# Kernel tuning notes

Hardware: AMD Instinct MI355X
Metric: run time of the kernel (lower is better)

## Reference

```python
import jax, jax.numpy as jnp
import numpy as np

B, T, F, H, S = 4096, 256, 64, 128, 32


def setup_inputs() -> dict:
    key = jax.random.key(0)
    ks = jax.random.split(key, 10)
    return {
        "x": jax.random.normal(ks[0], (B, T, F), jnp.float32),
        "static": jax.random.normal(ks[1], (B, S), jnp.float32),
        "hs0": jax.random.normal(ks[2], (B, H), jnp.float32),
        "cs0": jax.random.normal(ks[3], (B, H), jnp.float32),
        "W_ih": jax.random.normal(ks[4], (4 * H, F), jnp.float32) * 0.1,
        "W_hh": jax.random.normal(ks[5], (4 * H, H), jnp.float32) * 0.1,
        "b_ih": jax.random.normal(ks[6], (4 * H,), jnp.float32) * 0.1,
        "b_hh": jax.random.normal(ks[7], (4 * H,), jnp.float32) * 0.1,
        "W_lin": jax.random.normal(ks[8], (1, H + S), jnp.float32) * 0.1,
        "b_lin": jax.random.normal(ks[9], (1,), jnp.float32) * 0.1,
    }


def reference(x, static, hs0, cs0, W_ih, W_hh, b_ih, b_hh, W_lin, b_lin):
    # x: [B, T, F] -> time-major [T, B, F]; precompute input projections for all steps
    xs = jnp.swapaxes(x, 0, 1)
    px = jnp.einsum('tbf,gf->tbg', xs, W_ih) + b_ih  # [T, B, 4H]

    def step(carry, px_t):
        h, c = carry
        gates = px_t + h @ W_hh.T + b_hh  # [B, 4H]
        i, f, g, o = jnp.split(gates, 4, axis=-1)  # PyTorch LSTM gate order
        i = jax.nn.sigmoid(i)
        f = jax.nn.sigmoid(f)
        g = jnp.tanh(g)
        o = jax.nn.sigmoid(o)
        c = f * c + i * g
        h = o * jnp.tanh(c)
        return (h, c), None

    (h, c), _ = jax.lax.scan(step, (hs0, cs0), px)
    full = jnp.concatenate([h, static], axis=1)  # [B, H+S]
    return full @ W_lin.T + b_lin  # [B, 1]
```

## Files before the change

### kernel.cpp

```cpp
#include <hip/hip_runtime.h>
#include <hip/hip_bf16.h>

#define B_ 4096
#define T_ 256
#define F_ 64
#define H_ 128
#define S_ 32

typedef __attribute__((ext_vector_type(8))) short bf16x8;
typedef __attribute__((ext_vector_type(4))) float f32x4;

#define K1f (-1.4426950408889634f)
#define K2f (-2.8853900817779268f)

#define MF(A, B, C) __builtin_amdgcn_mfma_f32_16x16x32_bf16((A), (B), (C), 0, 0, 0)

__device__ __forceinline__ float bf2f(unsigned short u) {
    unsigned v = (unsigned)u << 16;
    return __builtin_bit_cast(float, v);
}
__device__ __forceinline__ short f2bs(float f) {
    return (short)__bfloat16_as_ushort(__float2bfloat16(f));
}

#define PHASE(HR, HW, XW, XN, TLD)                                               \
  {                                                                              \
    const char* hr_ = (const char*)(HR);                                         \
    bf16x8 a0 = *(const bf16x8*)(hr_ + fh0);                                     \
    bf16x8 a1 = *(const bf16x8*)(hr_ + fh1);                                     \
    bf16x8 a2 = *(const bf16x8*)(hr_ + fh2);                                     \
    bf16x8 a3 = *(const bf16x8*)(hr_ + fh3);                                     \
                    \
    { __hip_bfloat162 qx = __float22bfloat162_rn(xheld);                         \
      *(__hip_bfloat162*)((char*)(XW) + xws) = qx; }                             \
    xheld = *(const float2*)(gxs + (size_t)(TLD) * F_);                          \
                                          \
    f32x4 ac0 = sd0, ac1 = sd1, ac2 = sd2, ac3 = sd3;                            \
    ac0 = MF(wf[0][2], a0, ac0); ac1 = MF(wf[1][2], a0, ac1);                    \
    ac2 = MF(wf[2][2], a0, ac2); ac3 = MF(wf[3][2], a0, ac3);                    \
    ac0 = MF(wf[0][3], a1, ac0); ac1 = MF(wf[1][3], a1, ac1);                    \
    ac2 = MF(wf[2][3], a1, ac2); ac3 = MF(wf[3][3], a1, ac3);                    \
    ac0 = MF(wf[0][4], a2, ac0); ac1 = MF(wf[1][4], a2, ac1);                    \
    ac2 = MF(wf[2][4], a2, ac2); ac3 = MF(wf[3][4], a2, ac3);                    \
    ac0 = MF(wf[0][5], a3, ac0); ac1 = MF(wf[1][5], a3, ac1);                    \
    ac2 = MF(wf[2][5], a3, ac2); ac3 = MF(wf[3][5], a3, ac3);                    \
                                  \
    float hn[4];                                                                 \
    _Pragma("unroll")                                                            \
    for (int q = 0; q < 4; ++q) {                                                \
      const float ea = __builtin_amdgcn_exp2f(__builtin_fmaf(ac0[q], K1f, bs0[q])); \
      const float ef = __builtin_amdgcn_exp2f(__builtin_fmaf(ac1[q], K1f, bs1[q])); \
      const float eg = __builtin_amdgcn_exp2f(__builtin_fmaf(ac2[q], K2f, btn[q])); \
      const float eo = __builtin_amdgcn_exp2f(__builtin_fmaf(ac3[q], K1f, bs3[q])); \
      const float r1 = __builtin_amdgcn_rcpf(1.0f + ef);                         \
      const float r2 = __builtin_amdgcn_rcpf((1.0f + ea) * (1.0f + eg));         \
      const float cn = __builtin_fmaf(c[q], r1, (1.0f - eg) * r2);               \
      c[q] = cn;                                                                 \
      const float cc = fmaxf(cn, -30.0f);                                        \
      const float ec = __builtin_amdgcn_exp2f(cc * K2f);                         \
      const float r3 = __builtin_amdgcn_rcpf((1.0f + eo) * (1.0f + ec));         \
      hn[q] = (1.0f - ec) * r3;                                                  \
    }                                                                            \
    { float2 p0; p0.x = hn[0]; p0.y = hn[1];                                     \
      float2 p1; p1.x = hn[2]; p1.y = hn[3];                                     \
      __hip_bfloat162 b01 = __float22bfloat162_rn(p0);                           \
      __hip_bfloat162 b23 = __float22bfloat162_rn(p1);                           \
      uint2 uv; uv.x = *(unsigned*)&b01; uv.y = *(unsigned*)&b23;                \
      *(uint2*)((char*)(HW) + hwb) = uv; }                                       \
              \
    { const char* xn_ = (const char*)(XN);                                       \
      bf16x8 nf0 = *(const bf16x8*)(xn_ + fx0);                                  \
      bf16x8 nf1 = *(const bf16x8*)(xn_ + fx1);                                  \
      sd0 = MF(wf[0][0], nf0, z4); sd1 = MF(wf[1][0], nf0, z4);                  \
      sd2 = MF(wf[2][0], nf0, z4); sd3 = MF(wf[3][0], nf0, z4);                  \
      sd0 = MF(wf[0][1], nf1, sd0); sd1 = MF(wf[1][1], nf1, sd1);                \
      sd2 = MF(wf[2][1], nf1, sd2); sd3 = MF(wf[3][1], nf1, sd3); }              \
    asm volatile("s_waitcnt lgkmcnt(0)" ::: "memory");                           \
    __builtin_amdgcn_s_barrier();                                                \
  }

__global__ __launch_bounds__(512, 2) void lstm_fused_kernel(
    const float* __restrict__ x,
    const float* __restrict__ statik,
    const float* __restrict__ hs0,
    const float* __restrict__ cs0,
    const float* __restrict__ W_ih,
    const float* __restrict__ W_hh,
    const float* __restrict__ b_ih,
    const float* __restrict__ b_hh,
    const float* __restrict__ W_lin,
    const float* __restrict__ b_lin,
    float* __restrict__ out)
{
    __shared__ __align__(16) unsigned short h_l[2][16 * 128];
    __shared__ __align__(16) unsigned short x_l[4][16 * 64];

    const int tid  = threadIdx.x;
    const int lane = tid & 63;
    const int w    = tid >> 6;
    const int b0   = blockIdx.x * 16;

    if (w >= 4) __builtin_amdgcn_s_setprio(1);

    const int lrow = lane & 15;
    const int lkb  = lane >> 4;
    const int n0q  = w * 16 + lkb * 4;

    bf16x8 wf[4][6];
    #pragma unroll
    for (int g = 0; g < 4; ++g) {
        const int n = g * 128 + w * 16 + lrow;
        #pragma unroll
        for (int kt = 0; kt < 6; ++kt) {
            const int k0 = kt * 32 + lkb * 8;
            const float* src = (kt < 2) ? (W_ih + n * F_ + k0)
                                        : (W_hh + n * H_ + (k0 - 64));
            const float4 s0 = *(const float4*)(src);
            const float4 s1 = *(const float4*)(src + 4);
            bf16x8 v;
            v[0] = f2bs(s0.x); v[1] = f2bs(s0.y); v[2] = f2bs(s0.z); v[3] = f2bs(s0.w);
            v[4] = f2bs(s1.x); v[5] = f2bs(s1.y); v[6] = f2bs(s1.z); v[7] = f2bs(s1.w);
            wf[g][kt] = v;
        }
    }

    float bs0[4], bs1[4], btn[4], bs3[4];
    #pragma unroll
    for (int g = 0; g < 4; ++g) {
        const float4 bi = *(const float4*)(b_ih + g * 128 + n0q);
        const float4 bh = *(const float4*)(b_hh + g * 128 + n0q);
        const float bq[4] = {bi.x + bh.x, bi.y + bh.y, bi.z + bh.z, bi.w + bh.w};
        #pragma unroll
        for (int q = 0; q < 4; ++q) {
            if (g == 0)      bs0[q] = bq[q] * K1f;
            else if (g == 1) bs1[q] = bq[q] * K1f;
            else if (g == 2) btn[q] = bq[q] * K2f;
            else             bs3[q] = bq[q] * K1f;
        }
    }

    float c[4];
    {
        const float4 cv = *(const float4*)(cs0 + (size_t)(b0 + lrow) * H_ + n0q);
        c[0] = cv.x; c[1] = cv.y; c[2] = cv.z; c[3] = cv.w;
    }

    const int fsw = (lrow & 7) << 4;
    const int fx0 = lrow * 128 + ((lkb * 16) ^ fsw);
    const int fx1 = lrow * 128 + ((64 + lkb * 16) ^ fsw);
    const int fh0 = lrow * 256 + ((0   + lkb * 16) ^ fsw);
    const int fh1 = lrow * 256 + ((64  + lkb * 16) ^ fsw);
    const int fh2 = lrow * 256 + ((128 + lkb * 16) ^ fsw);
    const int fh3 = lrow * 256 + ((192 + lkb * 16) ^ fsw);
    const int hwb = lrow * 256 + ((n0q * 2) ^ fsw);

    const int srow = tid >> 5;
    const int scp  = tid & 31;
    const int ssw  = (srow & 7) << 4;
    const int xws  = srow * 128 + ((scp * 4) ^ ssw);

    const float* gxs = x + (size_t)(b0 + srow) * (T_ * F_) + scp * 2;
    float2 xheld;
    {
        const float* hp = hs0 + (size_t)(b0 + srow) * H_ + scp * 2;
        const float2 hv0 = *(const float2*)(hp);
        const float2 hv1 = *(const float2*)(hp + 64);
        __hip_bfloat162 q0 = __float22bfloat162_rn(hv0);
        __hip_bfloat162 q1 = __float22bfloat162_rn(hv1);
        *(__hip_bfloat162*)((char*)h_l[0] + srow * 256 + ((scp * 4) ^ ssw))       = q0;
        *(__hip_bfloat162*)((char*)h_l[0] + srow * 256 + ((128 + scp * 4) ^ ssw)) = q1;

        const float2 x0 = *(const float2*)(gxs);
        const float2 x1 = *(const float2*)(gxs + F_);
        __hip_bfloat162 qa = __float22bfloat162_rn(x0);
        __hip_bfloat162 qb = __float22bfloat162_rn(x1);
        *(__hip_bfloat162*)((char*)x_l[0] + xws) = qa;
        *(__hip_bfloat162*)((char*)x_l[1] + xws) = qb;
        xheld = *(const float2*)(gxs + 2 * F_);
    }
    __syncthreads();

    const f32x4 z4 = {0.0f, 0.0f, 0.0f, 0.0f};

    f32x4 sd0, sd1, sd2, sd3;
    {
        const char* xn_ = (const char*)x_l[0];
        bf16x8 nf0 = *(const bf16x8*)(xn_ + fx0);
        bf16x8 nf1 = *(const bf16x8*)(xn_ + fx1);
        sd0 = MF(wf[0][0], nf0, z4); sd1 = MF(wf[1][0], nf0, z4);
        sd2 = MF(wf[2][0], nf0, z4); sd3 = MF(wf[3][0], nf0, z4);
        sd0 = MF(wf[0][1], nf1, sd0); sd1 = MF(wf[1][1], nf1, sd1);
        sd2 = MF(wf[2][1], nf1, sd2); sd3 = MF(wf[3][1], nf1, sd3);
    }

    for (int t = 0; t < T_; t += 4) {
        const int t3 = (t + 3 < T_) ? t + 3 : T_ - 1;
        const int t4 = (t + 4 < T_) ? t + 4 : T_ - 1;
        const int t5 = (t + 5 < T_) ? t + 5 : T_ - 1;
        const int t6 = (t + 6 < T_) ? t + 6 : T_ - 1;
        PHASE(h_l[0], h_l[1], x_l[2], x_l[1], t3);
        PHASE(h_l[1], h_l[0], x_l[3], x_l[2], t4);
        PHASE(h_l[0], h_l[1], x_l[0], x_l[3], t5);
        PHASE(h_l[1], h_l[0], x_l[1], x_l[0], t6);
    }

    __builtin_amdgcn_s_setprio(0);

    {
        const char* hf = (const char*)h_l[0];
        const float wl0 = W_lin[lane];
        const float wl1 = W_lin[64 + lane];
        const float wl2 = (lane < S_) ? W_lin[128 + lane] : 0.0f;
        const float bl  = b_lin[0];
        #pragma unroll
        for (int rr = 0; rr < 2; ++rr) {
            const int r  = w * 2 + rr;
            const int rs = (r & 7) << 4;
            const unsigned short h0 =
                *(const unsigned short*)(hf + r * 256 + ((2 * lane) ^ rs));
            const unsigned short h1 =
                *(const unsigned short*)(hf + r * 256 + ((128 + 2 * lane) ^ rs));
            float p = bf2f(h0) * wl0 + bf2f(h1) * wl1;
            if (lane < S_) p += statik[(size_t)(b0 + r) * S_ + lane] * wl2;
            #pragma unroll
            for (int m = 32; m > 0; m >>= 1) p += __shfl_xor(p, m, 64);
            if (lane == 0) out[b0 + r] = p + bl;
        }
    }
}

extern "C" void kernel_launch(void* const* d_in, const int* in_sizes, int n_in,
                              void* d_out, int out_size, void* d_ws, size_t ws_size,
                              hipStream_t stream) {
    const float* x     = (const float*)d_in[0];
    const float* st    = (const float*)d_in[1];
    const float* hs0   = (const float*)d_in[2];
    const float* cs0   = (const float*)d_in[3];
    const float* W_ih  = (const float*)d_in[4];
    const float* W_hh  = (const float*)d_in[5];
    const float* b_ih  = (const float*)d_in[6];
    const float* b_hh  = (const float*)d_in[7];
    const float* W_lin = (const float*)d_in[8];
    const float* b_lin = (const float*)d_in[9];
    float* out = (float*)d_out;

    lstm_fused_kernel<<<dim3(B_ / 16), dim3(512), 0, stream>>>(
        x, st, hs0, cs0, W_ih, W_hh, b_ih, b_hh, W_lin, b_lin, out);
}
```

Measured before the change: 246.9 us.

## Split warps into two phase orderings to stagger MFMA and activation work

Waves 0-3 keep the original order (h MFMAs, activations, then next-step x seeds), while waves 4-7 compute the next-step x seed MFMAs first, before the h MFMAs and activations. The wave priority boost for the upper half is dropped. The aim is for the two groups of waves to hit the matrix unit and the transcendental/VALU work at different times within each barrier interval, so the pipes are shared better. It costs an extra set of four accumulator registers for the odd path and duplicates the loop code, which may add register pressure at 512 threads and 2 blocks per CU.

After: 261.5 us. 5.9% more time.

```diff
diff --git a/kernel.cpp b/kernel.cpp
--- a/kernel.cpp
+++ b/kernel.cpp
@@ -23,61 +23,86 @@
     return (short)__bfloat16_as_ushort(__float2bfloat16(f));
 }
 
-#define PHASE(HR, HW, XW, XN, TLD)                                               \
-  {                                                                              \
-    const char* hr_ = (const char*)(HR);                                         \
-    bf16x8 a0 = *(const bf16x8*)(hr_ + fh0);                                     \
-    bf16x8 a1 = *(const bf16x8*)(hr_ + fh1);                                     \
-    bf16x8 a2 = *(const bf16x8*)(hr_ + fh2);                                     \
-    bf16x8 a3 = *(const bf16x8*)(hr_ + fh3);                                     \
-                    \
-    { __hip_bfloat162 qx = __float22bfloat162_rn(xheld);                         \
-      *(__hip_bfloat162*)((char*)(XW) + xws) = qx; }                             \
-    xheld = *(const float2*)(gxs + (size_t)(TLD) * F_);                          \
-                                          \
-    f32x4 ac0 = sd0, ac1 = sd1, ac2 = sd2, ac3 = sd3;                            \
-    ac0 = MF(wf[0][2], a0, ac0); ac1 = MF(wf[1][2], a0, ac1);                    \
-    ac2 = MF(wf[2][2], a0, ac2); ac3 = MF(wf[3][2], a0, ac3);                    \
-    ac0 = MF(wf[0][3], a1, ac0); ac1 = MF(wf[1][3], a1, ac1);                    \
-    ac2 = MF(wf[2][3], a1, ac2); ac3 = MF(wf[3][3], a1, ac3);                    \
-    ac0 = MF(wf[0][4], a2, ac0); ac1 = MF(wf[1][4], a2, ac1);                    \
-    ac2 = MF(wf[2][4], a2, ac2); ac3 = MF(wf[3][4], a2, ac3);                    \
-    ac0 = MF(wf[0][5], a3, ac0); ac1 = MF(wf[1][5], a3, ac1);                    \
-    ac2 = MF(wf[2][5], a3, ac2); ac3 = MF(wf[3][5], a3, ac3);                    \
-                                  \
-    float hn[4];                                                                 \
-    _Pragma("unroll")                                                            \
-    for (int q = 0; q < 4; ++q) {                                                \
+
+#define STAGE_X(XW, TLD) \
+    { __hip_bfloat162 qx_ = __float22bfloat162_rn(xheld); \
+      *(__hip_bfloat162*)((char*)(XW) + xws) = qx_; } \
+    xheld = *(const float2*)(gxs + (size_t)(TLD) * F_);
+
+#define HMFMA16() \
+    ac0 = MF(wf[0][2], a0, ac0); ac1 = MF(wf[1][2], a0, ac1); \
+    ac2 = MF(wf[2][2], a0, ac2); ac3 = MF(wf[3][2], a0, ac3); \
+    ac0 = MF(wf[0][3], a1, ac0); ac1 = MF(wf[1][3], a1, ac1); \
+    ac2 = MF(wf[2][3], a1, ac2); ac3 = MF(wf[3][3], a1, ac3); \
+    ac0 = MF(wf[0][4], a2, ac0); ac1 = MF(wf[1][4], a2, ac1); \
+    ac2 = MF(wf[2][4], a2, ac2); ac3 = MF(wf[3][4], a2, ac3); \
+    ac0 = MF(wf[0][5], a3, ac0); ac1 = MF(wf[1][5], a3, ac1); \
+    ac2 = MF(wf[2][5], a3, ac2); ac3 = MF(wf[3][5], a3, ac3);
+
+#define SEEDS8(D0, D1, D2, D3, XN) \
+    { const char* xn_ = (const char*)(XN); \
+      bf16x8 nf0 = *(const bf16x8*)(xn_ + fx0); \
+      bf16x8 nf1 = *(const bf16x8*)(xn_ + fx1); \
+      D0 = MF(wf[0][0], nf0, z4);  D1 = MF(wf[1][0], nf0, z4); \
+      D2 = MF(wf[2][0], nf0, z4);  D3 = MF(wf[3][0], nf0, z4); \
+      D0 = MF(wf[0][1], nf1, D0);  D1 = MF(wf[1][1], nf1, D1); \
+      D2 = MF(wf[2][1], nf1, D2);  D3 = MF(wf[3][1], nf1, D3); }
+
+#define ACT_WRITE(HW) \
+    { float hn[4]; \
+    _Pragma("unroll") \
+    for (int q = 0; q < 4; ++q) { \
       const float ea = __builtin_amdgcn_exp2f(__builtin_fmaf(ac0[q], K1f, bs0[q])); \
       const float ef = __builtin_amdgcn_exp2f(__builtin_fmaf(ac1[q], K1f, bs1[q])); \
       const float eg = __builtin_amdgcn_exp2f(__builtin_fmaf(ac2[q], K2f, btn[q])); \
       const float eo = __builtin_amdgcn_exp2f(__builtin_fmaf(ac3[q], K1f, bs3[q])); \
-      const float r1 = __builtin_amdgcn_rcpf(1.0f + ef);                         \
-      const float r2 = __builtin_amdgcn_rcpf((1.0f + ea) * (1.0f + eg));         \
-      const float cn = __builtin_fmaf(c[q], r1, (1.0f - eg) * r2);               \
-      c[q] = cn;                                                                 \
-      const float cc = fmaxf(cn, -30.0f);                                        \
-      const float ec = __builtin_amdgcn_exp2f(cc * K2f);                         \
-      const float r3 = __builtin_amdgcn_rcpf((1.0f + eo) * (1.0f + ec));         \
-      hn[q] = (1.0f - ec) * r3;                                                  \
-    }                                                                            \
-    { float2 p0; p0.x = hn[0]; p0.y = hn[1];                                     \
-      float2 p1; p1.x = hn[2]; p1.y = hn[3];                                     \
-      __hip_bfloat162 b01 = __float22bfloat162_rn(p0);                           \
-      __hip_bfloat162 b23 = __float22bfloat162_rn(p1);                           \
-      uint2 uv; uv.x = *(unsigned*)&b01; uv.y = *(unsigned*)&b23;                \
-      *(uint2*)((char*)(HW) + hwb) = uv; }                                       \
-              \
-    { const char* xn_ = (const char*)(XN);                                       \
-      bf16x8 nf0 = *(const bf16x8*)(xn_ + fx0);                                  \
-      bf16x8 nf1 = *(const bf16x8*)(xn_ + fx1);                                  \
-      sd0 = MF(wf[0][0], nf0, z4); sd1 = MF(wf[1][0], nf0, z4);                  \
-      sd2 = MF(wf[2][0], nf0, z4); sd3 = MF(wf[3][0], nf0, z4);                  \
-      sd0 = MF(wf[0][1], nf1, sd0); sd1 = MF(wf[1][1], nf1, sd1);                \
-      sd2 = MF(wf[2][1], nf1, sd2); sd3 = MF(wf[3][1], nf1, sd3); }              \
-    asm volatile("s_waitcnt lgkmcnt(0)" ::: "memory");                           \
-    __builtin_amdgcn_s_barrier();                                                \
-  }
+      const float r1 = __builtin_amdgcn_rcpf(1.0f + ef); \
+      const float r2 = __builtin_amdgcn_rcpf((1.0f + ea) * (1.0f + eg)); \
+      const float cn = __builtin_fmaf(c[q], r1, (1.0f - eg) * r2); \
+      c[q] = cn; \
+      const float cc = fmaxf(cn, -30.0f); \
+      const float ec = __builtin_amdgcn_exp2f(cc * K2f); \
+      const float r3 = __builtin_amdgcn_rcpf((1.0f + eo) * (1.0f + ec)); \
+      hn[q] = (1.0f - ec) * r3; \
+    } \
+    { float2 p0; p0.x = hn[0]; p0.y = hn[1]; \
+      float2 p1; p1.x = hn[2]; p1.y = hn[3]; \
+      __hip_bfloat162 b01 = __float22bfloat162_rn(p0); \
+      __hip_bfloat162 b23 = __float22bfloat162_rn(p1); \
+      uint2 uv; uv.x = *(unsigned*)&b01; uv.y = *(unsigned*)&b23; \
+      *(uint2*)((char*)(HW) + hwb) = uv; } }
+
+#define ENDBAR() \
+    asm volatile("s_waitcnt lgkmcnt(0)" ::: "memory"); \
+    __builtin_amdgcn_s_barrier();
+
+#define PHASE_E(HR, HW, XW, XN, TLD) \
+  { const char* hr_ = (const char*)(HR); \
+    bf16x8 a0 = *(const bf16x8*)(hr_ + fh0); \
+    bf16x8 a1 = *(const bf16x8*)(hr_ + fh1); \
+    bf16x8 a2 = *(const bf16x8*)(hr_ + fh2); \
+    bf16x8 a3 = *(const bf16x8*)(hr_ + fh3); \
+    STAGE_X(XW, TLD); \
+    f32x4 ac0 = sd0, ac1 = sd1, ac2 = sd2, ac3 = sd3; \
+    HMFMA16(); \
+    ACT_WRITE(HW); \
+    SEEDS8(sd0, sd1, sd2, sd3, XN); \
+    ENDBAR(); }
+
+#define PHASE_O(HR, HW, XW, XN, TLD) \
+  { f32x4 sn0, sn1, sn2, sn3; \
+    SEEDS8(sn0, sn1, sn2, sn3, XN); \
+    STAGE_X(XW, TLD); \
+    const char* hr_ = (const char*)(HR); \
+    bf16x8 a0 = *(const bf16x8*)(hr_ + fh0); \
+    bf16x8 a1 = *(const bf16x8*)(hr_ + fh1); \
+    bf16x8 a2 = *(const bf16x8*)(hr_ + fh2); \
+    bf16x8 a3 = *(const bf16x8*)(hr_ + fh3); \
+    f32x4 ac0 = sd0, ac1 = sd1, ac2 = sd2, ac3 = sd3; \
+    HMFMA16(); \
+    ACT_WRITE(HW); \
+    sd0 = sn0; sd1 = sn1; sd2 = sn2; sd3 = sn3; \
+    ENDBAR(); }
 
 __global__ __launch_bounds__(512, 2) void lstm_fused_kernel(
     const float* __restrict__ x,
@@ -100,8 +125,6 @@
     const int w    = tid >> 6;
     const int b0   = blockIdx.x * 16;
 
-    if (w >= 4) __builtin_amdgcn_s_setprio(1);
-
     const int lrow = lane & 15;
     const int lkb  = lane >> 4;
     const int n0q  = w * 16 + lkb * 4;
@@ -183,28 +206,32 @@
     const f32x4 z4 = {0.0f, 0.0f, 0.0f, 0.0f};
 
     f32x4 sd0, sd1, sd2, sd3;
-    {
-        const char* xn_ = (const char*)x_l[0];
-        bf16x8 nf0 = *(const bf16x8*)(xn_ + fx0);
-        bf16x8 nf1 = *(const bf16x8*)(xn_ + fx1);
-        sd0 = MF(wf[0][0], nf0, z4); sd1 = MF(wf[1][0], nf0, z4);
-        sd2 = MF(wf[2][0], nf0, z4); sd3 = MF(wf[3][0], nf0, z4);
-        sd0 = MF(wf[0][1], nf1, sd0); sd1 = MF(wf[1][1], nf1, sd1);
-        sd2 = MF(wf[2][1], nf1, sd2); sd3 = MF(wf[3][1], nf1, sd3);
-    }
-
-    for (int t = 0; t < T_; t += 4) {
-        const int t3 = (t + 3 < T_) ? t + 3 : T_ - 1;
-        const int t4 = (t + 4 < T_) ? t + 4 : T_ - 1;
-        const int t5 = (t + 5 < T_) ? t + 5 : T_ - 1;
-        const int t6 = (t + 6 < T_) ? t + 6 : T_ - 1;
-        PHASE(h_l[0], h_l[1], x_l[2], x_l[1], t3);
-        PHASE(h_l[1], h_l[0], x_l[3], x_l[2], t4);
-        PHASE(h_l[0], h_l[1], x_l[0], x_l[3], t5);
-        PHASE(h_l[1], h_l[0], x_l[1], x_l[0], t6);
-    }
-
-    __builtin_amdgcn_s_setprio(0);
+    SEEDS8(sd0, sd1, sd2, sd3, x_l[0]);
+    sd0 = sd0;
+
+    if (w >= 4) {
+        for (int t = 0; t < T_; t += 4) {
+            const int t3 = (t + 3 < T_) ? t + 3 : T_ - 1;
+            const int t4 = (t + 4 < T_) ? t + 4 : T_ - 1;
+            const int t5 = (t + 5 < T_) ? t + 5 : T_ - 1;
+            const int t6 = (t + 6 < T_) ? t + 6 : T_ - 1;
+            PHASE_O(h_l[0], h_l[1], x_l[2], x_l[1], t3);
+            PHASE_O(h_l[1], h_l[0], x_l[3], x_l[2], t4);
+            PHASE_O(h_l[0], h_l[1], x_l[0], x_l[3], t5);
+            PHASE_O(h_l[1], h_l[0], x_l[1], x_l[0], t6);
+        }
+    } else {
+        for (int t = 0; t < T_; t += 4) {
+            const int t3 = (t + 3 < T_) ? t + 3 : T_ - 1;
+            const int t4 = (t + 4 < T_) ? t + 4 : T_ - 1;
+            const int t5 = (t + 5 < T_) ? t + 5 : T_ - 1;
+            const int t6 = (t + 6 < T_) ? t + 6 : T_ - 1;
+            PHASE_E(h_l[0], h_l[1], x_l[2], x_l[1], t3);
+            PHASE_E(h_l[1], h_l[0], x_l[3], x_l[2], t4);
+            PHASE_E(h_l[0], h_l[1], x_l[0], x_l[3], t5);
+            PHASE_E(h_l[1], h_l[0], x_l[1], x_l[0], t6);
+        }
+    }
 
     {
         const char* hf = (const char*)h_l[0];
```
